# Kernel tuning notes

Hardware: AMD Instinct MI355X
Metric: run time of the kernel (lower is better)

Reference implementation:

```python
import jax, jax.numpy as jnp
import numpy as np

B, S, D, H = 2, 2048, 1024, 16
HD = D // H
SPARSITY = 0.5
NEG_INF = jnp.float32(-jnp.inf)


def setup_inputs() -> dict:
    key = jax.random.key(0)
    ks = jax.random.split(key, 12)
    s = 1.0 / np.sqrt(D)
    inp = {
        "query": jax.random.normal(ks[0], (B, S, D), jnp.float32),
        "key": jax.random.normal(ks[1], (B, S, D), jnp.float32),
        "value": jax.random.normal(ks[2], (B, S, D), jnp.float32),
        "Wq": jax.random.uniform(ks[3], (D, D), jnp.float32, -s, s),
        "bq": jax.random.uniform(ks[4], (D,), jnp.float32, -s, s),
        "Wk": jax.random.uniform(ks[5], (D, D), jnp.float32, -s, s),
        "bk": jax.random.uniform(ks[6], (D,), jnp.float32, -s, s),
        "Wv": jax.random.uniform(ks[7], (D, D), jnp.float32, -s, s),
        "bv": jax.random.uniform(ks[8], (D,), jnp.float32, -s, s),
        "Wo": jax.random.uniform(ks[9], (D, D), jnp.float32, -s, s),
        "bo": jax.random.uniform(ks[10], (D,), jnp.float32, -s, s),
    }
    return inp


def reference(query, key, value, Wq, bq, Wk, bk, Wv, bv, Wo, bo):
    b, sq, _ = query.shape
    sk = key.shape[1]
    # projections -> [b, h, s, hd]
    Q = (query @ Wq.T + bq).reshape(b, sq, H, HD).transpose(0, 2, 1, 3)
    K = (key @ Wk.T + bk).reshape(b, sk, H, HD).transpose(0, 2, 1, 3)
    V = (value @ Wv.T + bv).reshape(b, sk, H, HD).transpose(0, 2, 1, 3)
    scale = jnp.float32(HD ** -0.5)
    scores = jnp.einsum('bhqd,bhkd->bhqk', Q, K) * scale  # [b,h,sq,sk]
    # top-k sparsification: keep k largest scores per query row, rest -> -inf
    k = max(1, int(sk * (1.0 - SPARSITY)))
    topk_vals, _ = jax.lax.top_k(scores, k)
    thresh = topk_vals[..., -1:]  # k-th largest value per row
    scores = jnp.where(scores >= thresh, scores, NEG_INF)
    attn = jax.nn.softmax(scores, axis=-1)  # dropout p=0.0 -> identity
    out = jnp.einsum('bhqk,bhkd->bhqd', attn, V)
    out = out.transpose(0, 2, 1, 3).reshape(b, sq, D)
    out = out @ Wo.T + bo
    return out, attn
```

## Files before the change

kernel.cpp:

```cpp
#include <hip/hip_runtime.h>
#include <math.h>

#define Bb 2
#define Ss 2048
#define Dd 1024
#define Hh 16
#define HDd 64
#define KSEL 1024
#define MROWS 4096

__device__ __forceinline__ unsigned f2u(float f) {
    unsigned u = __float_as_uint(f);
    return (u & 0x80000000u) ? ~u : (u | 0x80000000u);
}

template <int TRANSPOSED>
__device__ __forceinline__ void gemm_body_1024(const float* __restrict__ X,
                                               const float* __restrict__ W,
                                               const float* __restrict__ bias,
                                               float* __restrict__ Y,
                                               int m0, int n0) {
    const int tid = threadIdx.x;
    const int tx = tid & 15, ty = tid >> 4;

    __shared__ __align__(16) float As[16][128];
    __shared__ __align__(16) float Bs[16][128];

    float acc[8][8];
#pragma unroll
    for (int i = 0; i < 8; ++i)
#pragma unroll
        for (int j = 0; j < 8; ++j) acc[i][j] = 0.f;

    for (int k0 = 0; k0 < 1024; k0 += 16) {
#pragma unroll
        for (int c = 0; c < 2; ++c) {
            int idx = tid + c * 256;
            int row = idx >> 2;
            int kq  = (idx & 3) << 2;
            float4 va = *(const float4*)&X[(size_t)(m0 + row) * 1024 + k0 + kq];
            As[kq + 0][row] = va.x; As[kq + 1][row] = va.y;
            As[kq + 2][row] = va.z; As[kq + 3][row] = va.w;
            float4 vb = *(const float4*)&W[(size_t)(n0 + row) * 1024 + k0 + kq];
            Bs[kq + 0][row] = vb.x; Bs[kq + 1][row] = vb.y;
            Bs[kq + 2][row] = vb.z; Bs[kq + 3][row] = vb.w;
        }
        __syncthreads();
#pragma unroll
        for (int kk = 0; kk < 16; ++kk) {
            float a[8], b[8];
            *(float4*)&a[0] = *(const float4*)&As[kk][ty * 4];
            *(float4*)&a[4] = *(const float4*)&As[kk][64 + ty * 4];
            *(float4*)&b[0] = *(const float4*)&Bs[kk][tx * 4];
            *(float4*)&b[4] = *(const float4*)&Bs[kk][64 + tx * 4];
#pragma unroll
            for (int i = 0; i < 8; ++i)
#pragma unroll
                for (int j = 0; j < 8; ++j) acc[i][j] = fmaf(a[i], b[j], acc[i][j]);
        }
        __syncthreads();
    }

#pragma unroll
    for (int i = 0; i < 8; ++i) {
        int m = m0 + ((i < 4) ? (ty * 4 + i) : (64 + ty * 4 + i - 4));
#pragma unroll
        for (int jq = 0; jq < 2; ++jq) {
            int n = n0 + jq * 64 + tx * 4;
            float4 bv = *(const float4*)&bias[n];
            float4 v;
            v.x = acc[i][jq * 4 + 0] + bv.x;
            v.y = acc[i][jq * 4 + 1] + bv.y;
            v.z = acc[i][jq * 4 + 2] + bv.z;
            v.w = acc[i][jq * 4 + 3] + bv.w;
            if (TRANSPOSED) {
                int bi = m >> 11, s = m & 2047;
                int h = n >> 6, d = n & 63;
                *(float4*)&Y[(((size_t)(bi * Hh + h)) * Ss + s) * HDd + d] = v;
            } else {
                *(float4*)&Y[(size_t)m * 1024 + n] = v;
            }
        }
    }
}

__global__ __launch_bounds__(256) void qkv_kernel(
    const float* __restrict__ q, const float* __restrict__ k, const float* __restrict__ v,
    const float* __restrict__ Wq, const float* __restrict__ Wk, const float* __restrict__ Wv,
    const float* __restrict__ bq, const float* __restrict__ bk, const float* __restrict__ bv,
    float* __restrict__ Qo, float* __restrict__ Ko, float* __restrict__ Vo) {
    int z = blockIdx.z;
    const float* X = (z == 0) ? q : ((z == 1) ? k : v);
    const float* W = (z == 0) ? Wq : ((z == 1) ? Wk : Wv);
    const float* bias = (z == 0) ? bq : ((z == 1) ? bk : bv);
    float* Y = (z == 0) ? Qo : ((z == 1) ? Ko : Vo);
    gemm_body_1024<1>(X, W, bias, Y, blockIdx.y * 128, blockIdx.x * 128);
}

__global__ __launch_bounds__(256) void outproj_kernel(
    const float* __restrict__ O, const float* __restrict__ Wo,
    const float* __restrict__ bo, float* __restrict__ Y) {
    gemm_body_1024<0>(O, Wo, bo, Y, blockIdx.y * 128, blockIdx.x * 128);
}

__global__ __launch_bounds__(256) void scores_kernel(const float* __restrict__ Q,
                                                     const float* __restrict__ Kd,
                                                     float* __restrict__ Sc) {
    const int tid = threadIdx.x;
    const int tx = tid & 15, ty = tid >> 4;
    const int z = blockIdx.z;
    const int m0 = blockIdx.y * 128;
    const int n0 = blockIdx.x * 128;
    const float* Qz = Q + (size_t)z * Ss * HDd;
    const float* Kz = Kd + (size_t)z * Ss * HDd;
    float* Cz = Sc + (size_t)z * Ss * Ss;

    __shared__ __align__(16) float As[16][128];
    __shared__ __align__(16) float Bs[16][128];

    float acc[8][8];
#pragma unroll
    for (int i = 0; i < 8; ++i)
#pragma unroll
        for (int j = 0; j < 8; ++j) acc[i][j] = 0.f;

    for (int k0 = 0; k0 < 64; k0 += 16) {
#pragma unroll
        for (int c = 0; c < 2; ++c) {
            int idx = tid + c * 256;
            int row = idx >> 2;
            int kq  = (idx & 3) << 2;
            float4 va = *(const float4*)&Qz[(size_t)(m0 + row) * 64 + k0 + kq];
            As[kq + 0][row] = va.x; As[kq + 1][row] = va.y;
            As[kq + 2][row] = va.z; As[kq + 3][row] = va.w;
            float4 vb = *(const float4*)&Kz[(size_t)(n0 + row) * 64 + k0 + kq];
            Bs[kq + 0][row] = vb.x; Bs[kq + 1][row] = vb.y;
            Bs[kq + 2][row] = vb.z; Bs[kq + 3][row] = vb.w;
        }
        __syncthreads();
#pragma unroll
        for (int kk = 0; kk < 16; ++kk) {
            float a[8], b[8];
            *(float4*)&a[0] = *(const float4*)&As[kk][ty * 4];
            *(float4*)&a[4] = *(const float4*)&As[kk][64 + ty * 4];
            *(float4*)&b[0] = *(const float4*)&Bs[kk][tx * 4];
            *(float4*)&b[4] = *(const float4*)&Bs[kk][64 + tx * 4];
#pragma unroll
            for (int i = 0; i < 8; ++i)
#pragma unroll
                for (int j = 0; j < 8; ++j) acc[i][j] = fmaf(a[i], b[j], acc[i][j]);
        }
        __syncthreads();
    }

#pragma unroll
    for (int i = 0; i < 8; ++i) {
        int m = m0 + ((i < 4) ? (ty * 4 + i) : (64 + ty * 4 + i - 4));
#pragma unroll
        for (int jq = 0; jq < 2; ++jq) {
            int n = n0 + jq * 64 + tx * 4;
            float4 v;
            v.x = acc[i][jq * 4 + 0] * 0.125f;
            v.y = acc[i][jq * 4 + 1] * 0.125f;
            v.z = acc[i][jq * 4 + 2] * 0.125f;
            v.w = acc[i][jq * 4 + 3] * 0.125f;
            *(float4*)&Cz[(size_t)m * Ss + n] = v;
        }
    }
}

__global__ __launch_bounds__(256) void topk_softmax_kernel(float* __restrict__ Sc) {
    const int tid = threadIdx.x;
    const int wv = tid >> 6;
    float* p = Sc + (size_t)blockIdx.x * Ss;

    __shared__ unsigned hist[4][256];
    __shared__ unsigned shist[256];
    __shared__ float red[256];
    __shared__ unsigned sel[2];

    float f[8];
    unsigned ubits[8];
#pragma unroll
    for (int j = 0; j < 8; ++j) {
        f[j] = p[tid + j * 256];
        ubits[j] = f2u(f[j]);
    }

    unsigned prefix = 0, rk = KSEL;
    for (int pass = 0; pass < 4; ++pass) {
        const int shift = 24 - pass * 8;
        hist[0][tid] = 0; hist[1][tid] = 0; hist[2][tid] = 0; hist[3][tid] = 0;
        __syncthreads();
#pragma unroll
        for (int j = 0; j < 8; ++j) {
            unsigned u = ubits[j];
            bool ok = (pass == 0) ? true : ((u >> (shift + 8)) == prefix);
            if (ok) atomicAdd(&hist[wv][(u >> shift) & 255u], 1u);
        }
        __syncthreads();
        shist[tid] = hist[0][tid] + hist[1][tid] + hist[2][tid] + hist[3][tid];
        __syncthreads();
        for (int off = 1; off < 256; off <<= 1) {
            unsigned a = shist[tid];
            unsigned b = (tid + off < 256) ? shist[tid + off] : 0u;
            __syncthreads();
            shist[tid] = a + b;
            __syncthreads();
        }
        unsigned Sn = (tid < 255) ? shist[tid + 1] : 0u;
        if (shist[tid] >= rk && Sn < rk) { sel[0] = (unsigned)tid; sel[1] = rk - Sn; }
        __syncthreads();
        prefix = (prefix << 8) | sel[0];
        rk = sel[1];
        __syncthreads();
    }
    const unsigned uth = prefix;

    float lm = -INFINITY;
#pragma unroll
    for (int j = 0; j < 8; ++j) lm = fmaxf(lm, f[j]);
    red[tid] = lm;
    __syncthreads();
    for (int off = 128; off > 0; off >>= 1) {
        if (tid < off) red[tid] = fmaxf(red[tid], red[tid + off]);
        __syncthreads();
    }
    const float mx = red[0];
    __syncthreads();

    float e[8];
    float ls = 0.f;
#pragma unroll
    for (int j = 0; j < 8; ++j) {
        float ev = (ubits[j] >= uth) ? __expf(f[j] - mx) : 0.f;
        e[j] = ev;
        ls += ev;
    }
    red[tid] = ls;
    __syncthreads();
    for (int off = 128; off > 0; off >>= 1) {
        if (tid < off) red[tid] += red[tid + off];
        __syncthreads();
    }
    const float inv = 1.f / red[0];

#pragma unroll
    for (int j = 0; j < 8; ++j) p[tid + j * 256] = e[j] * inv;
}

__global__ __launch_bounds__(256) void pv_kernel(const float* __restrict__ A,
                                                 const float* __restrict__ V,
                                                 float* __restrict__ O) {
    const int tid = threadIdx.x;
    const int tx = tid & 15, ty = tid >> 4;
    const int z = blockIdx.y;
    const int m0 = blockIdx.x * 128;
    const int bi = z >> 4, h = z & 15;
    const float* Az = A + (size_t)z * Ss * Ss;
    const float* Vz = V + (size_t)z * Ss * HDd;

    __shared__ __align__(16) float As[32][128];
    __shared__ __align__(16) float Bs[32][64];

    float acc[8][4];
#pragma unroll
    for (int i = 0; i < 8; ++i)
#pragma unroll
        for (int j = 0; j < 4; ++j) acc[i][j] = 0.f;

    for (int k0 = 0; k0 < Ss; k0 += 32) {
#pragma unroll
        for (int c = 0; c < 4; ++c) {
            int idx = tid + c * 256;
            int row = idx >> 3;
            int kq  = (idx & 7) << 2;
            float4 va = *(const float4*)&Az[(size_t)(m0 + row) * Ss + k0 + kq];
            As[kq + 0][row] = va.x; As[kq + 1][row] = va.y;
            As[kq + 2][row] = va.z; As[kq + 3][row] = va.w;
        }
#pragma unroll
        for (int c = 0; c < 2; ++c) {
            int idx = tid + c * 256;
            int kr = idx >> 4;
            int dq = (idx & 15) << 2;
            *(float4*)&Bs[kr][dq] = *(const float4*)&Vz[(size_t)(k0 + kr) * 64 + dq];
        }
        __syncthreads();
#pragma unroll
        for (int kk = 0; kk < 32; ++kk) {
            float a[8], b[4];
            *(float4*)&a[0] = *(const float4*)&As[kk][ty * 8];
            *(float4*)&a[4] = *(const float4*)&As[kk][ty * 8 + 4];
            *(float4*)&b[0] = *(const float4*)&Bs[kk][tx * 4];
#pragma unroll
            for (int i = 0; i < 8; ++i)
#pragma unroll
                for (int j = 0; j < 4; ++j) acc[i][j] = fmaf(a[i], b[j], acc[i][j]);
        }
        __syncthreads();
    }

#pragma unroll
    for (int i = 0; i < 8; ++i) {
        int srow = m0 + ty * 8 + i;
        float4 v = {acc[i][0], acc[i][1], acc[i][2], acc[i][3]};
        *(float4*)&O[((size_t)(bi * Ss + srow)) * Dd + h * 64 + tx * 4] = v;
    }
}

extern "C" void kernel_launch(void* const* d_in, const int* in_sizes, int n_in,
                              void* d_out, int out_size, void* d_ws, size_t ws_size,
                              hipStream_t stream) {
    const float* q  = (const float*)d_in[0];
    const float* k  = (const float*)d_in[1];
    const float* v  = (const float*)d_in[2];
    const float* Wq = (const float*)d_in[3];
    const float* bq = (const float*)d_in[4];
    const float* Wk = (const float*)d_in[5];
    const float* bk = (const float*)d_in[6];
    const float* Wv = (const float*)d_in[7];
    const float* bv = (const float*)d_in[8];
    const float* Wo = (const float*)d_in[9];
    const float* bo = (const float*)d_in[10];

    float* out  = (float*)d_out;
    float* attn = out + (size_t)Bb * Ss * Dd;

    float* ws = (float*)d_ws;
    const size_t SZ = (size_t)Bb * Ss * Dd;
    float* Qb = ws;
    float* Kb = ws + SZ;
    float* Vb = ws + 2 * SZ;
    float* Ob = ws + 3 * SZ;

    dim3 blk(256);

    qkv_kernel<<<dim3(8, 32, 3), blk, 0, stream>>>(q, k, v, Wq, Wk, Wv, bq, bk, bv, Qb, Kb, Vb);
    scores_kernel<<<dim3(16, 16, 32), blk, 0, stream>>>(Qb, Kb, attn);
    topk_softmax_kernel<<<dim3(65536), blk, 0, stream>>>(attn);
    pv_kernel<<<dim3(16, 32), blk, 0, stream>>>(attn, Vb, Ob);
    outproj_kernel<<<dim3(8, 32), blk, 0, stream>>>(Ob, Wo, bo, out);
}
```

Measured before the change: 1.769 ms.

## Fuse QK^T scores with top-k radix select and softmax in one kernel

Replaces the separate scores GEMM and per-row top-k/softmax kernels with one kernel. Each 512-thread block computes 16 full score rows in registers. It then runs a 12/10/10-bit radix select on an LDS histogram to find the per-row threshold and applies the masked softmax before writing attn once. This removes the write and reread of the 2048x2048 score matrix per head and one launch. In exchange it uses a large LDS footprint (128KB histogram), restages all of K per block of 16 rows, and adds many block-wide barriers.

```diff
diff --git a/kernel.cpp b/kernel.cpp
--- a/kernel.cpp
+++ b/kernel.cpp
@@ -103,150 +103,312 @@
     gemm_body_1024<0>(O, Wo, bo, Y, blockIdx.y * 128, blockIdx.x * 128);
 }
 
-__global__ __launch_bounds__(256) void scores_kernel(const float* __restrict__ Q,
-                                                     const float* __restrict__ Kd,
-                                                     float* __restrict__ Sc) {
-    const int tid = threadIdx.x;
-    const int tx = tid & 15, ty = tid >> 4;
-    const int z = blockIdx.z;
-    const int m0 = blockIdx.y * 128;
-    const int n0 = blockIdx.x * 128;
-    const float* Qz = Q + (size_t)z * Ss * HDd;
-    const float* Kz = Kd + (size_t)z * Ss * HDd;
-    float* Cz = Sc + (size_t)z * Ss * Ss;
-
-    __shared__ __align__(16) float As[16][128];
-    __shared__ __align__(16) float Bs[16][128];
-
-    float acc[8][8];
-#pragma unroll
-    for (int i = 0; i < 8; ++i)
-#pragma unroll
-        for (int j = 0; j < 8; ++j) acc[i][j] = 0.f;
-
-    for (int k0 = 0; k0 < 64; k0 += 16) {
-#pragma unroll
-        for (int c = 0; c < 2; ++c) {
-            int idx = tid + c * 256;
-            int row = idx >> 2;
-            int kq  = (idx & 3) << 2;
-            float4 va = *(const float4*)&Qz[(size_t)(m0 + row) * 64 + k0 + kq];
-            As[kq + 0][row] = va.x; As[kq + 1][row] = va.y;
-            As[kq + 2][row] = va.z; As[kq + 3][row] = va.w;
-            float4 vb = *(const float4*)&Kz[(size_t)(n0 + row) * 64 + k0 + kq];
-            Bs[kq + 0][row] = vb.x; Bs[kq + 1][row] = vb.y;
-            Bs[kq + 2][row] = vb.z; Bs[kq + 3][row] = vb.w;
+__global__ __launch_bounds__(512) void fused_scores_topk_kernel(
+    const float* __restrict__ Q, const float* __restrict__ Kd,
+    float* __restrict__ Attn) {
+    const int t = threadIdx.x;
+    const int bh = blockIdx.x >> 7;
+    const int s0 = (blockIdx.x & 127) * 16;
+    const float* Qz = Q + (size_t)bh * Ss * HDd;
+    const float* Kz = Kd + (size_t)bh * Ss * HDd;
+    float* Cz = Attn + (size_t)bh * Ss * Ss;
+
+    __shared__ __align__(16) unsigned hist[32768];
+    __shared__ __align__(16) float QT[1024];
+    __shared__ unsigned gs[2048];
+    __shared__ unsigned ggs[128];
+    __shared__ unsigned selA[8], rkA[8], selB[8], rkB[8];
+    __shared__ unsigned prefixR[16], rkR[16], uthR[16];
+    __shared__ float red2[512];
+    __shared__ float mxR[16], invR[16];
+
+    float* KTf = reinterpret_cast<float*>(hist);
+    float* scratch = reinterpret_cast<float*>(hist);
+
+#pragma unroll
+    for (int j = 0; j < 2; ++j) {
+        int idx = t + j * 512;
+        int r = idx >> 6, d = idx & 63;
+        QT[d * 16 + r] = Qz[(size_t)(s0 + r) * 64 + d] * 0.125f;
+    }
+    if (t < 16) { rkR[t] = KSEL; prefixR[t] = 0u; }
+
+    float acc[16][4];
+#pragma unroll
+    for (int r = 0; r < 16; ++r)
+#pragma unroll
+        for (int i = 0; i < 4; ++i) acc[r][i] = 0.f;
+
+    for (int dt = 0; dt < 4; ++dt) {
+        const int d0 = dt * 16;
+        __syncthreads();
+#pragma unroll
+        for (int j = 0; j < 16; ++j) {
+            int idx = t + j * 512;
+            int c = idx >> 2, m = idx & 3;
+            float4 kv = *(const float4*)&Kz[(size_t)c * 64 + d0 + m * 4];
+            KTf[(m * 4 + 0) * 2048 + c] = kv.x;
+            KTf[(m * 4 + 1) * 2048 + c] = kv.y;
+            KTf[(m * 4 + 2) * 2048 + c] = kv.z;
+            KTf[(m * 4 + 3) * 2048 + c] = kv.w;
         }
         __syncthreads();
 #pragma unroll
         for (int kk = 0; kk < 16; ++kk) {
-            float a[8], b[8];
-            *(float4*)&a[0] = *(const float4*)&As[kk][ty * 4];
-            *(float4*)&a[4] = *(const float4*)&As[kk][64 + ty * 4];
-            *(float4*)&b[0] = *(const float4*)&Bs[kk][tx * 4];
-            *(float4*)&b[4] = *(const float4*)&Bs[kk][64 + tx * 4];
-#pragma unroll
-            for (int i = 0; i < 8; ++i)
-#pragma unroll
-                for (int j = 0; j < 8; ++j) acc[i][j] = fmaf(a[i], b[j], acc[i][j]);
-        }
-        __syncthreads();
-    }
-
-#pragma unroll
-    for (int i = 0; i < 8; ++i) {
-        int m = m0 + ((i < 4) ? (ty * 4 + i) : (64 + ty * 4 + i - 4));
-#pragma unroll
-        for (int jq = 0; jq < 2; ++jq) {
-            int n = n0 + jq * 64 + tx * 4;
-            float4 v;
-            v.x = acc[i][jq * 4 + 0] * 0.125f;
-            v.y = acc[i][jq * 4 + 1] * 0.125f;
-            v.z = acc[i][jq * 4 + 2] * 0.125f;
-            v.w = acc[i][jq * 4 + 3] * 0.125f;
-            *(float4*)&Cz[(size_t)m * Ss + n] = v;
-        }
-    }
-}
-
-__global__ __launch_bounds__(256) void topk_softmax_kernel(float* __restrict__ Sc) {
-    const int tid = threadIdx.x;
-    const int wv = tid >> 6;
-    float* p = Sc + (size_t)blockIdx.x * Ss;
-
-    __shared__ unsigned hist[4][256];
-    __shared__ unsigned shist[256];
-    __shared__ float red[256];
-    __shared__ unsigned sel[2];
-
-    float f[8];
-    unsigned ubits[8];
-#pragma unroll
-    for (int j = 0; j < 8; ++j) {
-        f[j] = p[tid + j * 256];
-        ubits[j] = f2u(f[j]);
-    }
-
-    unsigned prefix = 0, rk = KSEL;
-    for (int pass = 0; pass < 4; ++pass) {
-        const int shift = 24 - pass * 8;
-        hist[0][tid] = 0; hist[1][tid] = 0; hist[2][tid] = 0; hist[3][tid] = 0;
-        __syncthreads();
-#pragma unroll
-        for (int j = 0; j < 8; ++j) {
-            unsigned u = ubits[j];
-            bool ok = (pass == 0) ? true : ((u >> (shift + 8)) == prefix);
-            if (ok) atomicAdd(&hist[wv][(u >> shift) & 255u], 1u);
-        }
-        __syncthreads();
-        shist[tid] = hist[0][tid] + hist[1][tid] + hist[2][tid] + hist[3][tid];
-        __syncthreads();
-        for (int off = 1; off < 256; off <<= 1) {
-            unsigned a = shist[tid];
-            unsigned b = (tid + off < 256) ? shist[tid + off] : 0u;
-            __syncthreads();
-            shist[tid] = a + b;
-            __syncthreads();
-        }
-        unsigned Sn = (tid < 255) ? shist[tid + 1] : 0u;
-        if (shist[tid] >= rk && Sn < rk) { sel[0] = (unsigned)tid; sel[1] = rk - Sn; }
-        __syncthreads();
-        prefix = (prefix << 8) | sel[0];
-        rk = sel[1];
-        __syncthreads();
-    }
-    const unsigned uth = prefix;
-
-    float lm = -INFINITY;
-#pragma unroll
-    for (int j = 0; j < 8; ++j) lm = fmaxf(lm, f[j]);
-    red[tid] = lm;
-    __syncthreads();
-    for (int off = 128; off > 0; off >>= 1) {
-        if (tid < off) red[tid] = fmaxf(red[tid], red[tid + off]);
-        __syncthreads();
-    }
-    const float mx = red[0];
-    __syncthreads();
-
-    float e[8];
-    float ls = 0.f;
-#pragma unroll
-    for (int j = 0; j < 8; ++j) {
-        float ev = (ubits[j] >= uth) ? __expf(f[j] - mx) : 0.f;
-        e[j] = ev;
-        ls += ev;
-    }
-    red[tid] = ls;
-    __syncthreads();
-    for (int off = 128; off > 0; off >>= 1) {
-        if (tid < off) red[tid] += red[tid + off];
-        __syncthreads();
-    }
-    const float inv = 1.f / red[0];
-
-#pragma unroll
-    for (int j = 0; j < 8; ++j) p[tid + j * 256] = e[j] * inv;
+            float a[16], b[4];
+            *(float4*)&a[0]  = *(const float4*)&QT[(d0 + kk) * 16 + 0];
+            *(float4*)&a[4]  = *(const float4*)&QT[(d0 + kk) * 16 + 4];
+            *(float4*)&a[8]  = *(const float4*)&QT[(d0 + kk) * 16 + 8];
+            *(float4*)&a[12] = *(const float4*)&QT[(d0 + kk) * 16 + 12];
+            *(float4*)&b[0]  = *(const float4*)&KTf[kk * 2048 + 4 * t];
+#pragma unroll
+            for (int r = 0; r < 16; ++r)
+#pragma unroll
+                for (int i = 0; i < 4; ++i) acc[r][i] = fmaf(a[r], b[i], acc[r][i]);
+        }
+    }
+    __syncthreads();
+
+    uint4 zz; zz.x = 0u; zz.y = 0u; zz.z = 0u; zz.w = 0u;
+
+#pragma unroll
+    for (int g = 0; g < 2; ++g) {
+#pragma unroll
+        for (int j = 0; j < 16; ++j) *(uint4*)&hist[(t + j * 512) * 4] = zz;
+        __syncthreads();
+#pragma unroll
+        for (int r = 0; r < 8; ++r)
+#pragma unroll
+            for (int i = 0; i < 4; ++i) {
+                unsigned u = f2u(acc[g * 8 + r][i]);
+                atomicAdd(&hist[r * 4096 + (u >> 20)], 1u);
+            }
+        __syncthreads();
+#pragma unroll
+        for (int j = 0; j < 4; ++j) {
+            int idx = t + j * 512;
+            int r = idx >> 8, qq = idx & 255;
+            unsigned s = 0;
+            for (int i = 0; i < 16; ++i) s += hist[r * 4096 + qq * 16 + i];
+            gs[r * 256 + qq] = s;
+        }
+        __syncthreads();
+        if (t < 128) {
+            int r = t >> 4, qq = t & 15;
+            unsigned s = 0;
+            for (int i = 0; i < 16; ++i) s += gs[r * 256 + qq * 16 + i];
+            ggs[r * 16 + qq] = s;
+        }
+        __syncthreads();
+        if (t < 128) {
+            int r = t >> 4, j = t & 15;
+            unsigned rk = rkR[g * 8 + r];
+            unsigned suf = 0;
+            for (int i = j; i < 16; ++i) suf += ggs[r * 16 + i];
+            unsigned Sn = suf - ggs[r * 16 + j];
+            if (suf >= rk && Sn < rk) { selA[r] = (unsigned)j; rkA[r] = rk - Sn; }
+        }
+        __syncthreads();
+        if (t < 128) {
+            int r = t >> 4, j = t & 15;
+            unsigned rk = rkA[r];
+            int base = (int)selA[r] * 16;
+            unsigned suf = 0;
+            for (int i = j; i < 16; ++i) suf += gs[r * 256 + base + i];
+            unsigned Sn = suf - gs[r * 256 + base + j];
+            if (suf >= rk && Sn < rk) { selB[r] = (unsigned)(base + j); rkB[r] = rk - Sn; }
+        }
+        __syncthreads();
+        if (t < 128) {
+            int r = t >> 4, j = t & 15;
+            unsigned rk = rkB[r];
+            int base = (int)selB[r] * 16;
+            unsigned suf = 0;
+            for (int i = j; i < 16; ++i) suf += hist[r * 4096 + base + i];
+            unsigned Sn = suf - hist[r * 4096 + base + j];
+            if (suf >= rk && Sn < rk) {
+                prefixR[g * 8 + r] = (unsigned)(base + j);
+                rkR[g * 8 + r] = rk - Sn;
+            }
+        }
+        __syncthreads();
+
+#pragma unroll
+        for (int j = 0; j < 4; ++j) *(uint4*)&hist[(t + j * 512) * 4] = zz;
+        __syncthreads();
+#pragma unroll
+        for (int r = 0; r < 8; ++r) {
+            unsigned pr = prefixR[g * 8 + r];
+#pragma unroll
+            for (int i = 0; i < 4; ++i) {
+                unsigned u = f2u(acc[g * 8 + r][i]);
+                if ((u >> 20) == pr) atomicAdd(&hist[r * 1024 + ((u >> 10) & 1023u)], 1u);
+            }
+        }
+        __syncthreads();
+        {
+            int r = t >> 6, qq = t & 63;
+            unsigned s = 0;
+            for (int i = 0; i < 16; ++i) s += hist[r * 1024 + qq * 16 + i];
+            gs[r * 64 + qq] = s;
+        }
+        __syncthreads();
+        if (t < 128) {
+            int r = t >> 4, qq = t & 15;
+            unsigned s = 0;
+            for (int i = 0; i < 4; ++i) s += gs[r * 64 + qq * 4 + i];
+            ggs[r * 16 + qq] = s;
+        }
+        __syncthreads();
+        if (t < 128) {
+            int r = t >> 4, j = t & 15;
+            unsigned rk = rkR[g * 8 + r];
+            unsigned suf = 0;
+            for (int i = j; i < 16; ++i) suf += ggs[r * 16 + i];
+            unsigned Sn = suf - ggs[r * 16 + j];
+            if (suf >= rk && Sn < rk) { selA[r] = (unsigned)j; rkA[r] = rk - Sn; }
+        }
+        __syncthreads();
+        if (t < 32) {
+            int r = t >> 2, j = t & 3;
+            unsigned rk = rkA[r];
+            int base = (int)selA[r] * 4;
+            unsigned suf = 0;
+            for (int i = j; i < 4; ++i) suf += gs[r * 64 + base + i];
+            unsigned Sn = suf - gs[r * 64 + base + j];
+            if (suf >= rk && Sn < rk) { selB[r] = (unsigned)(base + j); rkB[r] = rk - Sn; }
+        }
+        __syncthreads();
+        if (t < 128) {
+            int r = t >> 4, j = t & 15;
+            unsigned rk = rkB[r];
+            int base = (int)selB[r] * 16;
+            unsigned suf = 0;
+            for (int i = j; i < 16; ++i) suf += hist[r * 1024 + base + i];
+            unsigned Sn = suf - hist[r * 1024 + base + j];
+            if (suf >= rk && Sn < rk) {
+                prefixR[g * 8 + r] = (prefixR[g * 8 + r] << 10) | (unsigned)(base + j);
+                rkR[g * 8 + r] = rk - Sn;
+            }
+        }
+        __syncthreads();
+
+#pragma unroll
+        for (int j = 0; j < 4; ++j) *(uint4*)&hist[(t + j * 512) * 4] = zz;
+        __syncthreads();
+#pragma unroll
+        for (int r = 0; r < 8; ++r) {
+            unsigned pr = prefixR[g * 8 + r];
+#pragma unroll
+            for (int i = 0; i < 4; ++i) {
+                unsigned u = f2u(acc[g * 8 + r][i]);
+                if ((u >> 10) == pr) atomicAdd(&hist[r * 1024 + (u & 1023u)], 1u);
+            }
+        }
+        __syncthreads();
+        {
+            int r = t >> 6, qq = t & 63;
+            unsigned s = 0;
+            for (int i = 0; i < 16; ++i) s += hist[r * 1024 + qq * 16 + i];
+            gs[r * 64 + qq] = s;
+        }
+        __syncthreads();
+        if (t < 128) {
+            int r = t >> 4, qq = t & 15;
+            unsigned s = 0;
+            for (int i = 0; i < 4; ++i) s += gs[r * 64 + qq * 4 + i];
+            ggs[r * 16 + qq] = s;
+        }
+        __syncthreads();
+        if (t < 128) {
+            int r = t >> 4, j = t & 15;
+            unsigned rk = rkR[g * 8 + r];
+            unsigned suf = 0;
+            for (int i = j; i < 16; ++i) suf += ggs[r * 16 + i];
+            unsigned Sn = suf - ggs[r * 16 + j];
+            if (suf >= rk && Sn < rk) { selA[r] = (unsigned)j; rkA[r] = rk - Sn; }
+        }
+        __syncthreads();
+        if (t < 32) {
+            int r = t >> 2, j = t & 3;
+            unsigned rk = rkA[r];
+            int base = (int)selA[r] * 4;
+            unsigned suf = 0;
+            for (int i = j; i < 4; ++i) suf += gs[r * 64 + base + i];
+            unsigned Sn = suf - gs[r * 64 + base + j];
+            if (suf >= rk && Sn < rk) { selB[r] = (unsigned)(base + j); rkB[r] = rk - Sn; }
+        }
+        __syncthreads();
+        if (t < 128) {
+            int r = t >> 4, j = t & 15;
+            unsigned rk = rkB[r];
+            int base = (int)selB[r] * 16;
+            unsigned suf = 0;
+            for (int i = j; i < 16; ++i) suf += hist[r * 1024 + base + i];
+            unsigned Sn = suf - hist[r * 1024 + base + j];
+            if (suf >= rk && Sn < rk)
+                uthR[g * 8 + r] = (prefixR[g * 8 + r] << 10) | (unsigned)(base + j);
+        }
+        __syncthreads();
+    }
+
+#pragma unroll
+    for (int r = 0; r < 16; ++r) {
+        float m = fmaxf(fmaxf(acc[r][0], acc[r][1]), fmaxf(acc[r][2], acc[r][3]));
+        scratch[r * 512 + t] = m;
+    }
+    __syncthreads();
+    {
+        int r = t >> 5, seg = t & 31;
+        float m = scratch[r * 512 + seg * 16];
+        for (int i = 1; i < 16; ++i) m = fmaxf(m, scratch[r * 512 + seg * 16 + i]);
+        red2[r * 32 + seg] = m;
+    }
+    __syncthreads();
+    if (t < 16) {
+        float m = red2[t * 32];
+        for (int i = 1; i < 32; ++i) m = fmaxf(m, red2[t * 32 + i]);
+        mxR[t] = m;
+    }
+    __syncthreads();
+
+#pragma unroll
+    for (int r = 0; r < 16; ++r) {
+        float mx = mxR[r];
+        unsigned uth = uthR[r];
+        float s = 0.f;
+#pragma unroll
+        for (int i = 0; i < 4; ++i) {
+            unsigned u = f2u(acc[r][i]);
+            float e = (u >= uth) ? __expf(acc[r][i] - mx) : 0.f;
+            acc[r][i] = e;
+            s += e;
+        }
+        scratch[r * 512 + t] = s;
+    }
+    __syncthreads();
+    {
+        int r = t >> 5, seg = t & 31;
+        float s = 0.f;
+        for (int i = 0; i < 16; ++i) s += scratch[r * 512 + seg * 16 + i];
+        red2[r * 32 + seg] = s;
+    }
+    __syncthreads();
+    if (t < 16) {
+        float s = 0.f;
+        for (int i = 0; i < 32; ++i) s += red2[t * 32 + i];
+        invR[t] = 1.f / s;
+    }
+    __syncthreads();
+
+#pragma unroll
+    for (int r = 0; r < 16; ++r) {
+        float inv = invR[r];
+        float4 o;
+        o.x = acc[r][0] * inv; o.y = acc[r][1] * inv;
+        o.z = acc[r][2] * inv; o.w = acc[r][3] * inv;
+        *(float4*)&Cz[(size_t)(s0 + r) * Ss + 4 * t] = o;
+    }
 }
 
 __global__ __launch_bounds__(256) void pv_kernel(const float* __restrict__ A,
@@ -337,8 +499,7 @@
     dim3 blk(256);
 
     qkv_kernel<<<dim3(8, 32, 3), blk, 0, stream>>>(q, k, v, Wq, Wk, Wv, bq, bk, bv, Qb, Kb, Vb);
-    scores_kernel<<<dim3(16, 16, 32), blk, 0, stream>>>(Qb, Kb, attn);
-    topk_softmax_kernel<<<dim3(65536), blk, 0, stream>>>(attn);
+    fused_scores_topk_kernel<<<dim3(4096), dim3(512), 0, stream>>>(Qb, Kb, attn);
     pv_kernel<<<dim3(16, 32), blk, 0, stream>>>(attn, Vb, Ob);
     outproj_kernel<<<dim3(8, 32), blk, 0, stream>>>(Ob, Wo, bo, out);
 }
```

Measured after the change: 1.989 ms. 1.12x slower.
